# Kernel tuning notes

Measured on AMD Instinct MI355X. Metric: run time of the kernel, lower is better.

The kernel has to match this reference:

```python
import jax, jax.numpy as jnp
import numpy as np

N, K, F = 20000, 32, 128
H, D = 4, 64            # heads, att_out_size
C = 40                  # num_classes
NEG_SLOPE = 0.2


def setup_inputs() -> dict:
    key = jax.random.key(0)
    ks = jax.random.split(key, 6)
    return {
        "node_feature": jax.random.normal(ks[0], (N, F), dtype=jnp.float32),
        "neighbor_nodes_feature": jax.random.normal(ks[1], (N, K, F), dtype=jnp.float32),
        "W": jax.random.normal(ks[2], (F, H * D), dtype=jnp.float32) / np.sqrt(F),
        "a_src": jax.random.normal(ks[3], (H, D), dtype=jnp.float32) / np.sqrt(D),
        "a_dst": jax.random.normal(ks[4], (H, D), dtype=jnp.float32) / np.sqrt(D),
        "weight": jax.random.normal(ks[5], (H * D, C), dtype=jnp.float32) / np.sqrt(H * D),
    }


def reference(node_feature, neighbor_nodes_feature, W, a_src, a_dst, weight):
    n = node_feature.shape[0]
    # Linear transform center nodes and neighbors, split heads
    h_i = (node_feature @ W).reshape(n, H, D)                     # [N,H,D]
    h_j = (neighbor_nodes_feature @ W).reshape(n, K, H, D)        # [N,K,H,D]
    # Attention logits: a_src . h_i + a_dst . h_j, LeakyReLU
    e_i = jnp.einsum('nhd,hd->nh', h_i, a_src)                    # [N,H]
    e_j = jnp.einsum('nkhd,hd->nkh', h_j, a_dst)                  # [N,K,H]
    e = jax.nn.leaky_relu(e_i[:, None, :] + e_j, NEG_SLOPE)       # [N,K,H]
    # Softmax over the K neighbors (segment softmax in dense form)
    alpha = jax.nn.softmax(e, axis=1)                             # [N,K,H]
    # Attention-weighted aggregation, concat heads
    out = jnp.einsum('nkh,nkhd->nhd', alpha, h_j).reshape(n, H * D)
    # Dense classifier (torch.mm)
    return out @ weight                                            # [N,C]
```

## Files before the change

kernel.cpp:

```cpp
#include <hip/hip_runtime.h>

#define KN 32
#define NF 128
#define NH 4
#define HD 256
#define NC 40
#define NPB 8
#define XSS 132

#define WS_WSRC 0
#define WS_WDST 512
#define WS_MT   1024
#define WS_EI   (1024 + NC * 512)

__global__ void gat_prep_wm(const float* __restrict__ W,
                            const float* __restrict__ a_src,
                            const float* __restrict__ a_dst,
                            const float* __restrict__ cls_w,
                            float* __restrict__ ws)
{
    if (blockIdx.x < 4) {
        int g = blockIdx.x * 256 + threadIdx.x;
        int which = g >> 9, h = (g >> 7) & 3, f = g & 127;
        const float* a = which ? a_dst : a_src;
        float s = 0.f;
        #pragma unroll 8
        for (int d = 0; d < 64; ++d)
            s = fmaf(W[f * HD + h * 64 + d], a[h * 64 + d], s);
        ws[g] = s;
    } else {
        int g = (blockIdx.x - 4) * 256 + threadIdx.x;
        if (g >= NC * 512) return;
        int cls = g >> 9, c = g & 511;
        int h = c >> 7, f = c & 127;
        float s = 0.f;
        #pragma unroll 8
        for (int d = 0; d < 64; ++d)
            s = fmaf(W[f * HD + h * 64 + d], cls_w[(h * 64 + d) * NC + cls], s);
        ws[WS_MT + (size_t)cls * 512 + c] = s;
    }
}

__global__ void gat_prep_ei(const float* __restrict__ nodef,
                            float* __restrict__ ws, int n_nodes)
{
    const int t = threadIdx.x;
    const int lane = t & 63;
    const int node = blockIdx.x * 64 + (t >> 6) * 16 + (lane >> 2);
    const int q = lane & 3;
    if (node >= n_nodes) return;
    const float* wsrc = ws + WS_WSRC;
    const float4* xp = (const float4*)(nodef + (size_t)node * NF + q * 32);
    float p0 = 0.f, p1 = 0.f, p2 = 0.f, p3 = 0.f;
    #pragma unroll
    for (int j = 0; j < 8; ++j) {
        float4 x  = xp[j];
        float4 w0 = *(const float4*)&wsrc[0 * NF + q * 32 + 4 * j];
        float4 w1 = *(const float4*)&wsrc[1 * NF + q * 32 + 4 * j];
        float4 w2 = *(const float4*)&wsrc[2 * NF + q * 32 + 4 * j];
        float4 w3 = *(const float4*)&wsrc[3 * NF + q * 32 + 4 * j];
        p0 += x.x*w0.x + x.y*w0.y + x.z*w0.z + x.w*w0.w;
        p1 += x.x*w1.x + x.y*w1.y + x.z*w1.z + x.w*w1.w;
        p2 += x.x*w2.x + x.y*w2.y + x.z*w2.z + x.w*w2.w;
        p3 += x.x*w3.x + x.y*w3.y + x.z*w3.z + x.w*w3.w;
    }
    #pragma unroll
    for (int st = 1; st < 4; st <<= 1) {
        p0 += __shfl_xor(p0, st); p1 += __shfl_xor(p1, st);
        p2 += __shfl_xor(p2, st); p3 += __shfl_xor(p3, st);
    }
    if (q == 0)
        *(float4*)&ws[WS_EI + (size_t)node * 4] = make_float4(p0, p1, p2, p3);
}

static __device__ __forceinline__ void lds_barrier() {
    __builtin_amdgcn_sched_barrier(0);
    asm volatile("s_waitcnt lgkmcnt(0)");
    __builtin_amdgcn_sched_barrier(0);
    __builtin_amdgcn_s_barrier();
    __builtin_amdgcn_sched_barrier(0);
}

__device__ __forceinline__ void gat_body(
    int i_, float* __restrict__ XsB, float* __restrict__ eB,
    float* __restrict__ zrow, float4 xv[4], const float4 wd[4][4],
    const float eiv[NPB], const float* __restrict__ neigh,
    int node0, int kq, int fq, int wv, int lane)
{
    #pragma unroll
    for (int j = 0; j < 4; ++j)
        *(float4*)&XsB[kq * XSS + fq * 4 + 32 * j] = xv[j];

    float s0 = 0.f, s1 = 0.f, s2 = 0.f, s3 = 0.f;
    #pragma unroll
    for (int j = 0; j < 4; ++j) {
        float4 x = xv[j];
        s0 += x.x*wd[0][j].x + x.y*wd[0][j].y + x.z*wd[0][j].z + x.w*wd[0][j].w;
        s1 += x.x*wd[1][j].x + x.y*wd[1][j].y + x.z*wd[1][j].z + x.w*wd[1][j].w;
        s2 += x.x*wd[2][j].x + x.y*wd[2][j].y + x.z*wd[2][j].z + x.w*wd[2][j].w;
        s3 += x.x*wd[3][j].x + x.y*wd[3][j].y + x.z*wd[3][j].z + x.w*wd[3][j].w;
    }

    if (i_ + 2 < NPB) {
        const float4* src = (const float4*)(neigh + ((size_t)(node0 + i_ + 2) * KN + kq) * NF);
        #pragma unroll
        for (int j = 0; j < 4; ++j) xv[j] = src[fq + 8 * j];
    }

    #pragma unroll
    for (int st = 1; st < 8; st <<= 1) {
        s0 += __shfl_xor(s0, st); s1 += __shfl_xor(s1, st);
        s2 += __shfl_xor(s2, st); s3 += __shfl_xor(s3, st);
    }
    if (fq == 0) {
        eB[0 * KN + kq] = s0; eB[1 * KN + kq] = s1;
        eB[2 * KN + kq] = s2; eB[3 * KN + kq] = s3;
    }

    lds_barrier();

    const float ei_h = eiv[i_];
    float ss = 0.f, zx = 0.f, zy = 0.f;
    #pragma unroll
    for (int m = 0; m < 8; ++m) {
        float4 evm = *(const float4*)&eB[wv * KN + m * 4];
        float el[4] = {evm.x, evm.y, evm.z, evm.w};
        #pragma unroll
        for (int kk = 0; kk < 4; ++kk) {
            float z_ = ei_h + el[kk];
            float l_ = fmaxf(z_, 0.2f * z_);
            float p_ = __expf(l_);
            ss += p_;
            float xa = XsB[(m * 4 + kk) * XSS + lane];
            float xb = XsB[(m * 4 + kk) * XSS + 64 + lane];
            zx = fmaf(p_, xa, zx);
            zy = fmaf(p_, xb, zy);
        }
    }
    float inv = 1.f / ss;
    zrow[wv * NF + lane]      = zx * inv;
    zrow[wv * NF + 64 + lane] = zy * inv;
}

__global__ __launch_bounds__(256, 3)
void gat_main(const float* __restrict__ neigh,
              const float* __restrict__ ws,
              float* __restrict__ out, int n_nodes)
{
    __shared__ __align__(16) float Xs[2][KN * XSS];
    __shared__ __align__(16) float zl[NPB][512];
    __shared__ __align__(16) float e_lds[2][NH * KN];

    const int t    = threadIdx.x;
    const int lane = t & 63;
    const int kq   = t >> 3;
    const int fq   = t & 7;
    const int wv   = t >> 6;
    const float* wdst = ws + WS_WDST;
    const float* MT   = ws + WS_MT;
    const float* ei_g = ws + WS_EI;

    const int node0 = blockIdx.x * NPB;
    if (node0 >= n_nodes) return;

    float4 wd[4][4];
    #pragma unroll
    for (int h = 0; h < 4; ++h)
        #pragma unroll
        for (int j = 0; j < 4; ++j)
            wd[h][j] = *(const float4*)&wdst[h * NF + fq * 4 + 32 * j];
    float eiv[NPB];
    #pragma unroll
    for (int i = 0; i < NPB; ++i)
        eiv[i] = ei_g[(size_t)(node0 + i) * 4 + wv];

    float4 xvA[4], xvB[4];
    {
        const float4* sA = (const float4*)(neigh + ((size_t)node0 * KN + kq) * NF);
        const float4* sB = (const float4*)(neigh + ((size_t)(node0 + 1) * KN + kq) * NF);
        #pragma unroll
        for (int j = 0; j < 4; ++j) { xvA[j] = sA[fq + 8 * j]; xvB[j] = sB[fq + 8 * j]; }
    }

    #pragma unroll
    for (int ii = 0; ii < NPB; ii += 2) {
        gat_body(ii,     Xs[0], e_lds[0], zl[ii],     xvA, wd, eiv, neigh,
                 node0, kq, fq, wv, lane);
        gat_body(ii + 1, Xs[1], e_lds[1], zl[ii + 1], xvB, wd, eiv, neigh,
                 node0, kq, fq, wv, lane);
    }
    __syncthreads();

    float* ypart = &Xs[0][0];
    {
        int cls = t & 63, s = t >> 6;
        if (cls < NC) {
            const float4* mp = (const float4*)&MT[(size_t)cls * 512 + s * 128];
            float acc[NPB];
            #pragma unroll
            for (int i = 0; i < NPB; ++i) acc[i] = 0.f;
            #pragma unroll 2
            for (int c4 = 0; c4 < 32; ++c4) {
                float4 mv = mp[c4];
                #pragma unroll
                for (int i = 0; i < NPB; ++i) {
                    float4 zv = *(const float4*)&zl[i][s * 128 + c4 * 4];
                    acc[i] += zv.x * mv.x + zv.y * mv.y + zv.z * mv.z + zv.w * mv.w;
                }
            }
            #pragma unroll
            for (int i = 0; i < NPB; ++i)
                ypart[s * (NPB * NC) + i * NC + cls] = acc[i];
        }
    }
    __syncthreads();
    #pragma unroll
    for (int rep = 0; rep < 2; ++rep) {
        int p = t + rep * 256;
        if (p < NPB * NC) {
            float y = ypart[p] + ypart[NPB * NC + p]
                    + ypart[2 * NPB * NC + p] + ypart[3 * NPB * NC + p];
            out[(size_t)node0 * NC + p] = y;
        }
    }
}

extern "C" void kernel_launch(void* const* d_in, const int* in_sizes, int n_in,
                              void* d_out, int out_size, void* d_ws, size_t ws_size,
                              hipStream_t stream) {
    const float* nodef = (const float*)d_in[0];
    const float* neigh = (const float*)d_in[1];
    const float* W     = (const float*)d_in[2];
    const float* a_src = (const float*)d_in[3];
    const float* a_dst = (const float*)d_in[4];
    const float* cls_w = (const float*)d_in[5];
    float* out = (float*)d_out;
    float* ws  = (float*)d_ws;

    const int n_nodes = in_sizes[0] / NF;

    hipLaunchKernelGGL(gat_prep_wm, dim3(4 + (NC * 512 + 255) / 256), dim3(256), 0, stream,
                       W, a_src, a_dst, cls_w, ws);
    hipLaunchKernelGGL(gat_prep_ei, dim3((n_nodes + 63) / 64), dim3(256), 0, stream,
                       nodef, ws, n_nodes);
    hipLaunchKernelGGL(gat_main, dim3((n_nodes + NPB - 1) / NPB), dim3(256), 0, stream,
                       neigh, ws, out, n_nodes);
}
```

Before: 125.6 us.

## Give each wavefront its own nodes and drop block-wide barriers in the main GAT loop

Restructures gat_main so each of the 4 wavefronts processes 8 nodes on its own (32 nodes per block). Neighbor rows are read straight from global memory twice, once for the logits and once for the aggregation, instead of being staged in LDS with block barriers. Softmax sums use in-wave shuffles, and the per-node aggregated features are stored in LDS as bf16 to fit 32 nodes before the classifier matmul. This removes per-node __syncthreads and LDS staging but doubles global/L2 reads of neighbor features and adds bf16 rounding error. The grid now assumes n_nodes is divisible by 32, which holds for 20000.

```diff
diff --git a/kernel.cpp b/kernel.cpp
--- a/kernel.cpp
+++ b/kernel.cpp
@@ -5,13 +5,23 @@
 #define NH 4
 #define HD 256
 #define NC 40
-#define NPB 8
-#define XSS 132
+#define NPW 8
+#define WPB 4
+#define NPB2 (NPW * WPB)
 
 #define WS_WSRC 0
 #define WS_WDST 512
 #define WS_MT   1024
 #define WS_EI   (1024 + NC * 512)
+
+static __device__ __forceinline__ unsigned short bf16_of(float x) {
+    union { float f; unsigned u; } v; v.f = x;
+    unsigned r = v.u + 0x7FFFu + ((v.u >> 16) & 1u);
+    return (unsigned short)(r >> 16);
+}
+static __device__ __forceinline__ float f_of_bf16(unsigned short b) {
+    union { unsigned u; float f; } v; v.u = ((unsigned)b) << 16; return v.f;
+}
 
 __global__ void gat_prep_wm(const float* __restrict__ W,
                             const float* __restrict__ a_src,
@@ -73,95 +83,25 @@
         *(float4*)&ws[WS_EI + (size_t)node * 4] = make_float4(p0, p1, p2, p3);
 }
 
-static __device__ __forceinline__ void lds_barrier() {
-    __builtin_amdgcn_sched_barrier(0);
-    asm volatile("s_waitcnt lgkmcnt(0)");
-    __builtin_amdgcn_sched_barrier(0);
-    __builtin_amdgcn_s_barrier();
-    __builtin_amdgcn_sched_barrier(0);
-}
-
-__device__ __forceinline__ void gat_body(
-    int i_, float* __restrict__ XsB, float* __restrict__ eB,
-    float* __restrict__ zrow, float4 xv[4], const float4 wd[4][4],
-    const float eiv[NPB], const float* __restrict__ neigh,
-    int node0, int kq, int fq, int wv, int lane)
-{
-    #pragma unroll
-    for (int j = 0; j < 4; ++j)
-        *(float4*)&XsB[kq * XSS + fq * 4 + 32 * j] = xv[j];
-
-    float s0 = 0.f, s1 = 0.f, s2 = 0.f, s3 = 0.f;
-    #pragma unroll
-    for (int j = 0; j < 4; ++j) {
-        float4 x = xv[j];
-        s0 += x.x*wd[0][j].x + x.y*wd[0][j].y + x.z*wd[0][j].z + x.w*wd[0][j].w;
-        s1 += x.x*wd[1][j].x + x.y*wd[1][j].y + x.z*wd[1][j].z + x.w*wd[1][j].w;
-        s2 += x.x*wd[2][j].x + x.y*wd[2][j].y + x.z*wd[2][j].z + x.w*wd[2][j].w;
-        s3 += x.x*wd[3][j].x + x.y*wd[3][j].y + x.z*wd[3][j].z + x.w*wd[3][j].w;
-    }
-
-    if (i_ + 2 < NPB) {
-        const float4* src = (const float4*)(neigh + ((size_t)(node0 + i_ + 2) * KN + kq) * NF);
-        #pragma unroll
-        for (int j = 0; j < 4; ++j) xv[j] = src[fq + 8 * j];
-    }
-
-    #pragma unroll
-    for (int st = 1; st < 8; st <<= 1) {
-        s0 += __shfl_xor(s0, st); s1 += __shfl_xor(s1, st);
-        s2 += __shfl_xor(s2, st); s3 += __shfl_xor(s3, st);
-    }
-    if (fq == 0) {
-        eB[0 * KN + kq] = s0; eB[1 * KN + kq] = s1;
-        eB[2 * KN + kq] = s2; eB[3 * KN + kq] = s3;
-    }
-
-    lds_barrier();
-
-    const float ei_h = eiv[i_];
-    float ss = 0.f, zx = 0.f, zy = 0.f;
-    #pragma unroll
-    for (int m = 0; m < 8; ++m) {
-        float4 evm = *(const float4*)&eB[wv * KN + m * 4];
-        float el[4] = {evm.x, evm.y, evm.z, evm.w};
-        #pragma unroll
-        for (int kk = 0; kk < 4; ++kk) {
-            float z_ = ei_h + el[kk];
-            float l_ = fmaxf(z_, 0.2f * z_);
-            float p_ = __expf(l_);
-            ss += p_;
-            float xa = XsB[(m * 4 + kk) * XSS + lane];
-            float xb = XsB[(m * 4 + kk) * XSS + 64 + lane];
-            zx = fmaf(p_, xa, zx);
-            zy = fmaf(p_, xb, zy);
-        }
-    }
-    float inv = 1.f / ss;
-    zrow[wv * NF + lane]      = zx * inv;
-    zrow[wv * NF + 64 + lane] = zy * inv;
-}
-
 __global__ __launch_bounds__(256, 3)
 void gat_main(const float* __restrict__ neigh,
               const float* __restrict__ ws,
               float* __restrict__ out, int n_nodes)
 {
-    __shared__ __align__(16) float Xs[2][KN * XSS];
-    __shared__ __align__(16) float zl[NPB][512];
-    __shared__ __align__(16) float e_lds[2][NH * KN];
+    __shared__ __align__(16) unsigned short zlB[NPB2][512];
+    __shared__ __align__(16) float alpha_l[WPB][2][KN * NH];
 
     const int t    = threadIdx.x;
+    const int w    = t >> 6;
     const int lane = t & 63;
-    const int kq   = t >> 3;
-    const int fq   = t & 7;
-    const int wv   = t >> 6;
+    const int g8   = lane >> 3;
+    const int fq   = lane & 7;
     const float* wdst = ws + WS_WDST;
     const float* MT   = ws + WS_MT;
     const float* ei_g = ws + WS_EI;
 
-    const int node0 = blockIdx.x * NPB;
-    if (node0 >= n_nodes) return;
+    const int node0  = blockIdx.x * NPB2;
+    const int nodeW0 = node0 + w * NPW;
 
     float4 wd[4][4];
     #pragma unroll
@@ -169,58 +109,120 @@
         #pragma unroll
         for (int j = 0; j < 4; ++j)
             wd[h][j] = *(const float4*)&wdst[h * NF + fq * 4 + 32 * j];
-    float eiv[NPB];
-    #pragma unroll
-    for (int i = 0; i < NPB; ++i)
-        eiv[i] = ei_g[(size_t)(node0 + i) * 4 + wv];
-
-    float4 xvA[4], xvB[4];
+
+    for (int i = 0; i < NPW; ++i) {
+        const int node = nodeW0 + i;
+        const float* xb = neigh + (size_t)node * (KN * NF);
+        const float4 eis = *(const float4*)&ei_g[(size_t)node * 4];
+
+        float ep[4][4];
+        #pragma unroll
+        for (int r8 = 0; r8 < 4; ++r8) {
+            const float4* xr = (const float4*)(xb + (size_t)(r8 * 8 + g8) * NF);
+            float4 x0 = xr[fq], x1 = xr[fq + 8], x2 = xr[fq + 16], x3 = xr[fq + 24];
+            #pragma unroll
+            for (int h = 0; h < 4; ++h) {
+                ep[r8][h] =
+                    x0.x*wd[h][0].x + x0.y*wd[h][0].y + x0.z*wd[h][0].z + x0.w*wd[h][0].w
+                  + x1.x*wd[h][1].x + x1.y*wd[h][1].y + x1.z*wd[h][1].z + x1.w*wd[h][1].w
+                  + x2.x*wd[h][2].x + x2.y*wd[h][2].y + x2.z*wd[h][2].z + x2.w*wd[h][2].w
+                  + x3.x*wd[h][3].x + x3.y*wd[h][3].y + x3.z*wd[h][3].z + x3.w*wd[h][3].w;
+            }
+        }
+        #pragma unroll
+        for (int st = 1; st < 8; st <<= 1)
+            #pragma unroll
+            for (int r8 = 0; r8 < 4; ++r8)
+                #pragma unroll
+                for (int h = 0; h < 4; ++h)
+                    ep[r8][h] += __shfl_xor(ep[r8][h], st);
+
+        const float eh[4] = {eis.x, eis.y, eis.z, eis.w};
+        float ex[4][4], ssh[4] = {0.f, 0.f, 0.f, 0.f};
+        #pragma unroll
+        for (int r8 = 0; r8 < 4; ++r8)
+            #pragma unroll
+            for (int h = 0; h < 4; ++h) {
+                float z = eh[h] + ep[r8][h];
+                float l = fmaxf(z, 0.2f * z);
+                ex[r8][h] = __expf(l);
+                ssh[h] += ex[r8][h];
+            }
+        #pragma unroll
+        for (int st = 8; st < 64; st <<= 1)
+            #pragma unroll
+            for (int h = 0; h < 4; ++h)
+                ssh[h] += __shfl_xor(ssh[h], st);
+        float inv[4];
+        #pragma unroll
+        for (int h = 0; h < 4; ++h) inv[h] = 1.f / ssh[h];
+
+        float* al = &alpha_l[w][i & 1][0];
+        if (fq == 0) {
+            #pragma unroll
+            for (int r8 = 0; r8 < 4; ++r8)
+                *(float4*)&al[(r8 * 8 + g8) * 4] =
+                    make_float4(ex[r8][0], ex[r8][1], ex[r8][2], ex[r8][3]);
+        }
+        asm volatile("s_waitcnt lgkmcnt(0)" ::: "memory");
+        __builtin_amdgcn_sched_barrier(0);
+
+        float zA[4] = {0.f, 0.f, 0.f, 0.f}, zB[4] = {0.f, 0.f, 0.f, 0.f};
+        const float* xcol = xb + lane * 2;
+        #pragma unroll 8
+        for (int k = 0; k < KN; ++k) {
+            float4 a4 = *(const float4*)&al[k * 4];
+            float2 x2 = *(const float2*)(xcol + (size_t)k * NF);
+            zA[0] = fmaf(a4.x, x2.x, zA[0]); zB[0] = fmaf(a4.x, x2.y, zB[0]);
+            zA[1] = fmaf(a4.y, x2.x, zA[1]); zB[1] = fmaf(a4.y, x2.y, zB[1]);
+            zA[2] = fmaf(a4.z, x2.x, zA[2]); zB[2] = fmaf(a4.z, x2.y, zB[2]);
+            zA[3] = fmaf(a4.w, x2.x, zA[3]); zB[3] = fmaf(a4.w, x2.y, zB[3]);
+        }
+        unsigned short* zr = zlB[w * NPW + i];
+        #pragma unroll
+        for (int h = 0; h < 4; ++h) {
+            ushort2 p;
+            p.x = bf16_of(zA[h] * inv[h]);
+            p.y = bf16_of(zB[h] * inv[h]);
+            *(ushort2*)&zr[h * NF + lane * 2] = p;
+        }
+    }
+    __syncthreads();
+
     {
-        const float4* sA = (const float4*)(neigh + ((size_t)node0 * KN + kq) * NF);
-        const float4* sB = (const float4*)(neigh + ((size_t)(node0 + 1) * KN + kq) * NF);
-        #pragma unroll
-        for (int j = 0; j < 4; ++j) { xvA[j] = sA[fq + 8 * j]; xvB[j] = sB[fq + 8 * j]; }
-    }
-
-    #pragma unroll
-    for (int ii = 0; ii < NPB; ii += 2) {
-        gat_body(ii,     Xs[0], e_lds[0], zl[ii],     xvA, wd, eiv, neigh,
-                 node0, kq, fq, wv, lane);
-        gat_body(ii + 1, Xs[1], e_lds[1], zl[ii + 1], xvB, wd, eiv, neigh,
-                 node0, kq, fq, wv, lane);
-    }
-    __syncthreads();
-
-    float* ypart = &Xs[0][0];
-    {
-        int cls = t & 63, s = t >> 6;
+        const int cls = t & 63, s = t >> 6;
+        float acc[NPB2];
         if (cls < NC) {
             const float4* mp = (const float4*)&MT[(size_t)cls * 512 + s * 128];
-            float acc[NPB];
-            #pragma unroll
-            for (int i = 0; i < NPB; ++i) acc[i] = 0.f;
+            #pragma unroll
+            for (int i = 0; i < NPB2; ++i) acc[i] = 0.f;
             #pragma unroll 2
             for (int c4 = 0; c4 < 32; ++c4) {
                 float4 mv = mp[c4];
                 #pragma unroll
-                for (int i = 0; i < NPB; ++i) {
-                    float4 zv = *(const float4*)&zl[i][s * 128 + c4 * 4];
-                    acc[i] += zv.x * mv.x + zv.y * mv.y + zv.z * mv.z + zv.w * mv.w;
+                for (int i = 0; i < NPB2; ++i) {
+                    ushort4 zv = *(const ushort4*)&zlB[i][s * 128 + c4 * 4];
+                    acc[i] += f_of_bf16(zv.x) * mv.x + f_of_bf16(zv.y) * mv.y
+                            + f_of_bf16(zv.z) * mv.z + f_of_bf16(zv.w) * mv.w;
                 }
             }
-            #pragma unroll
-            for (int i = 0; i < NPB; ++i)
-                ypart[s * (NPB * NC) + i * NC + cls] = acc[i];
-        }
-    }
-    __syncthreads();
-    #pragma unroll
-    for (int rep = 0; rep < 2; ++rep) {
-        int p = t + rep * 256;
-        if (p < NPB * NC) {
-            float y = ypart[p] + ypart[NPB * NC + p]
-                    + ypart[2 * NPB * NC + p] + ypart[3 * NPB * NC + p];
-            out[(size_t)node0 * NC + p] = y;
+        }
+        __syncthreads();
+        float* ypart = (float*)&zlB[0][0];
+        if (cls < NC) {
+            #pragma unroll
+            for (int i = 0; i < NPB2; ++i)
+                ypart[s * (NPB2 * NC) + i * NC + cls] = acc[i];
+        }
+        __syncthreads();
+        #pragma unroll
+        for (int rep = 0; rep < 5; ++rep) {
+            int p = t + rep * 256;
+            if (p < NPB2 * NC) {
+                float y = ypart[p] + ypart[NPB2 * NC + p]
+                        + ypart[2 * NPB2 * NC + p] + ypart[3 * NPB2 * NC + p];
+                out[(size_t)node0 * NC + p] = y;
+            }
         }
     }
 }
@@ -243,6 +245,6 @@
                        W, a_src, a_dst, cls_w, ws);
     hipLaunchKernelGGL(gat_prep_ei, dim3((n_nodes + 63) / 64), dim3(256), 0, stream,
                        nodef, ws, n_nodes);
-    hipLaunchKernelGGL(gat_main, dim3((n_nodes + NPB - 1) / NPB), dim3(256), 0, stream,
+    hipLaunchKernelGGL(gat_main, dim3(n_nodes / NPB2), dim3(256), 0, stream,
                        neigh, ws, out, n_nodes);
 }
```

Result: slower. 178.3 us (+41.9%).

## Fuse center-node logit prep into main kernel and deepen neighbor prefetch to three

Applied to the files above, without the earlier changes.

Removes the separate gat_prep_ei launch and its workspace round-trip. Each block now computes its eight center-node source logits directly into LDS with a 32-lane shuffle reduction. The main loop changes from a paired two-node body to a single loop that keeps three nodes' neighbor rows in registers, so loads are issued three iterations ahead. LDS reads of X and writes of z switch to float2 with an interleaved column mapping. The trade-off is more VGPRs for the extra prefetch set, which could limit occupancy.

```diff
diff --git a/kernel.cpp b/kernel.cpp
--- a/kernel.cpp
+++ b/kernel.cpp
@@ -11,7 +11,6 @@
 #define WS_WSRC 0
 #define WS_WDST 512
 #define WS_MT   1024
-#define WS_EI   (1024 + NC * 512)
 
 __global__ void gat_prep_wm(const float* __restrict__ W,
                             const float* __restrict__ a_src,
@@ -41,38 +40,6 @@
     }
 }
 
-__global__ void gat_prep_ei(const float* __restrict__ nodef,
-                            float* __restrict__ ws, int n_nodes)
-{
-    const int t = threadIdx.x;
-    const int lane = t & 63;
-    const int node = blockIdx.x * 64 + (t >> 6) * 16 + (lane >> 2);
-    const int q = lane & 3;
-    if (node >= n_nodes) return;
-    const float* wsrc = ws + WS_WSRC;
-    const float4* xp = (const float4*)(nodef + (size_t)node * NF + q * 32);
-    float p0 = 0.f, p1 = 0.f, p2 = 0.f, p3 = 0.f;
-    #pragma unroll
-    for (int j = 0; j < 8; ++j) {
-        float4 x  = xp[j];
-        float4 w0 = *(const float4*)&wsrc[0 * NF + q * 32 + 4 * j];
-        float4 w1 = *(const float4*)&wsrc[1 * NF + q * 32 + 4 * j];
-        float4 w2 = *(const float4*)&wsrc[2 * NF + q * 32 + 4 * j];
-        float4 w3 = *(const float4*)&wsrc[3 * NF + q * 32 + 4 * j];
-        p0 += x.x*w0.x + x.y*w0.y + x.z*w0.z + x.w*w0.w;
-        p1 += x.x*w1.x + x.y*w1.y + x.z*w1.z + x.w*w1.w;
-        p2 += x.x*w2.x + x.y*w2.y + x.z*w2.z + x.w*w2.w;
-        p3 += x.x*w3.x + x.y*w3.y + x.z*w3.z + x.w*w3.w;
-    }
-    #pragma unroll
-    for (int st = 1; st < 4; st <<= 1) {
-        p0 += __shfl_xor(p0, st); p1 += __shfl_xor(p1, st);
-        p2 += __shfl_xor(p2, st); p3 += __shfl_xor(p3, st);
-    }
-    if (q == 0)
-        *(float4*)&ws[WS_EI + (size_t)node * 4] = make_float4(p0, p1, p2, p3);
-}
-
 static __device__ __forceinline__ void lds_barrier() {
     __builtin_amdgcn_sched_barrier(0);
     asm volatile("s_waitcnt lgkmcnt(0)");
@@ -81,113 +48,120 @@
     __builtin_amdgcn_sched_barrier(0);
 }
 
-__device__ __forceinline__ void gat_body(
-    int i_, float* __restrict__ XsB, float* __restrict__ eB,
-    float* __restrict__ zrow, float4 xv[4], const float4 wd[4][4],
-    const float eiv[NPB], const float* __restrict__ neigh,
-    int node0, int kq, int fq, int wv, int lane)
-{
-    #pragma unroll
-    for (int j = 0; j < 4; ++j)
-        *(float4*)&XsB[kq * XSS + fq * 4 + 32 * j] = xv[j];
-
-    float s0 = 0.f, s1 = 0.f, s2 = 0.f, s3 = 0.f;
-    #pragma unroll
-    for (int j = 0; j < 4; ++j) {
-        float4 x = xv[j];
-        s0 += x.x*wd[0][j].x + x.y*wd[0][j].y + x.z*wd[0][j].z + x.w*wd[0][j].w;
-        s1 += x.x*wd[1][j].x + x.y*wd[1][j].y + x.z*wd[1][j].z + x.w*wd[1][j].w;
-        s2 += x.x*wd[2][j].x + x.y*wd[2][j].y + x.z*wd[2][j].z + x.w*wd[2][j].w;
-        s3 += x.x*wd[3][j].x + x.y*wd[3][j].y + x.z*wd[3][j].z + x.w*wd[3][j].w;
-    }
-
-    if (i_ + 2 < NPB) {
-        const float4* src = (const float4*)(neigh + ((size_t)(node0 + i_ + 2) * KN + kq) * NF);
-        #pragma unroll
-        for (int j = 0; j < 4; ++j) xv[j] = src[fq + 8 * j];
-    }
-
-    #pragma unroll
-    for (int st = 1; st < 8; st <<= 1) {
-        s0 += __shfl_xor(s0, st); s1 += __shfl_xor(s1, st);
-        s2 += __shfl_xor(s2, st); s3 += __shfl_xor(s3, st);
-    }
-    if (fq == 0) {
-        eB[0 * KN + kq] = s0; eB[1 * KN + kq] = s1;
-        eB[2 * KN + kq] = s2; eB[3 * KN + kq] = s3;
-    }
-
-    lds_barrier();
-
-    const float ei_h = eiv[i_];
-    float ss = 0.f, zx = 0.f, zy = 0.f;
-    #pragma unroll
-    for (int m = 0; m < 8; ++m) {
-        float4 evm = *(const float4*)&eB[wv * KN + m * 4];
-        float el[4] = {evm.x, evm.y, evm.z, evm.w};
-        #pragma unroll
-        for (int kk = 0; kk < 4; ++kk) {
-            float z_ = ei_h + el[kk];
-            float l_ = fmaxf(z_, 0.2f * z_);
-            float p_ = __expf(l_);
-            ss += p_;
-            float xa = XsB[(m * 4 + kk) * XSS + lane];
-            float xb = XsB[(m * 4 + kk) * XSS + 64 + lane];
-            zx = fmaf(p_, xa, zx);
-            zy = fmaf(p_, xb, zy);
-        }
-    }
-    float inv = 1.f / ss;
-    zrow[wv * NF + lane]      = zx * inv;
-    zrow[wv * NF + 64 + lane] = zy * inv;
-}
-
 __global__ __launch_bounds__(256, 3)
-void gat_main(const float* __restrict__ neigh,
+void gat_main(const float* __restrict__ nodef,
+              const float* __restrict__ neigh,
               const float* __restrict__ ws,
               float* __restrict__ out, int n_nodes)
 {
     __shared__ __align__(16) float Xs[2][KN * XSS];
     __shared__ __align__(16) float zl[NPB][512];
     __shared__ __align__(16) float e_lds[2][NH * KN];
+    __shared__ __align__(16) float ei_lds[NPB][NH];
 
     const int t    = threadIdx.x;
     const int lane = t & 63;
     const int kq   = t >> 3;
     const int fq   = t & 7;
     const int wv   = t >> 6;
+    const float* wsrc = ws + WS_WSRC;
     const float* wdst = ws + WS_WDST;
     const float* MT   = ws + WS_MT;
-    const float* ei_g = ws + WS_EI;
 
     const int node0 = blockIdx.x * NPB;
     if (node0 >= n_nodes) return;
 
+    {
+        const int i2 = t >> 5, sub = t & 31;
+        float4 x = ((const float4*)(nodef + (size_t)(node0 + i2) * NF))[sub];
+        float4 w0 = *(const float4*)&wsrc[0 * NF + sub * 4];
+        float4 w1 = *(const float4*)&wsrc[1 * NF + sub * 4];
+        float4 w2 = *(const float4*)&wsrc[2 * NF + sub * 4];
+        float4 w3 = *(const float4*)&wsrc[3 * NF + sub * 4];
+        float p0 = x.x*w0.x + x.y*w0.y + x.z*w0.z + x.w*w0.w;
+        float p1 = x.x*w1.x + x.y*w1.y + x.z*w1.z + x.w*w1.w;
+        float p2 = x.x*w2.x + x.y*w2.y + x.z*w2.z + x.w*w2.w;
+        float p3 = x.x*w3.x + x.y*w3.y + x.z*w3.z + x.w*w3.w;
+        #pragma unroll
+        for (int st = 1; st < 32; st <<= 1) {
+            p0 += __shfl_xor(p0, st); p1 += __shfl_xor(p1, st);
+            p2 += __shfl_xor(p2, st); p3 += __shfl_xor(p3, st);
+        }
+        if (sub == 0)
+            *(float4*)&ei_lds[i2][0] = make_float4(p0, p1, p2, p3);
+    }
+
     float4 wd[4][4];
     #pragma unroll
     for (int h = 0; h < 4; ++h)
         #pragma unroll
         for (int j = 0; j < 4; ++j)
             wd[h][j] = *(const float4*)&wdst[h * NF + fq * 4 + 32 * j];
-    float eiv[NPB];
-    #pragma unroll
-    for (int i = 0; i < NPB; ++i)
-        eiv[i] = ei_g[(size_t)(node0 + i) * 4 + wv];
-
-    float4 xvA[4], xvB[4];
-    {
-        const float4* sA = (const float4*)(neigh + ((size_t)node0 * KN + kq) * NF);
-        const float4* sB = (const float4*)(neigh + ((size_t)(node0 + 1) * KN + kq) * NF);
-        #pragma unroll
-        for (int j = 0; j < 4; ++j) { xvA[j] = sA[fq + 8 * j]; xvB[j] = sB[fq + 8 * j]; }
-    }
-
-    #pragma unroll
-    for (int ii = 0; ii < NPB; ii += 2) {
-        gat_body(ii,     Xs[0], e_lds[0], zl[ii],     xvA, wd, eiv, neigh,
-                 node0, kq, fq, wv, lane);
-        gat_body(ii + 1, Xs[1], e_lds[1], zl[ii + 1], xvB, wd, eiv, neigh,
-                 node0, kq, fq, wv, lane);
+
+    float4 xv[3][4];
+    #pragma unroll
+    for (int s = 0; s < 3; ++s) {
+        const float4* src = (const float4*)(neigh + ((size_t)(node0 + s) * KN + kq) * NF);
+        #pragma unroll
+        for (int j = 0; j < 4; ++j) xv[s][j] = src[fq + 8 * j];
+    }
+
+    #pragma unroll
+    for (int i = 0; i < NPB; ++i) {
+        const int set = i % 3;
+        const int buf = i & 1;
+
+        #pragma unroll
+        for (int j = 0; j < 4; ++j)
+            *(float4*)&Xs[buf][kq * XSS + fq * 4 + 32 * j] = xv[set][j];
+
+        float s0 = 0.f, s1 = 0.f, s2 = 0.f, s3 = 0.f;
+        #pragma unroll
+        for (int j = 0; j < 4; ++j) {
+            float4 x = xv[set][j];
+            s0 += x.x*wd[0][j].x + x.y*wd[0][j].y + x.z*wd[0][j].z + x.w*wd[0][j].w;
+            s1 += x.x*wd[1][j].x + x.y*wd[1][j].y + x.z*wd[1][j].z + x.w*wd[1][j].w;
+            s2 += x.x*wd[2][j].x + x.y*wd[2][j].y + x.z*wd[2][j].z + x.w*wd[2][j].w;
+            s3 += x.x*wd[3][j].x + x.y*wd[3][j].y + x.z*wd[3][j].z + x.w*wd[3][j].w;
+        }
+
+        if (i + 3 < NPB) {
+            const float4* src = (const float4*)(neigh + ((size_t)(node0 + i + 3) * KN + kq) * NF);
+            #pragma unroll
+            for (int j = 0; j < 4; ++j) xv[set][j] = src[fq + 8 * j];
+        }
+
+        #pragma unroll
+        for (int st = 1; st < 8; st <<= 1) {
+            s0 += __shfl_xor(s0, st); s1 += __shfl_xor(s1, st);
+            s2 += __shfl_xor(s2, st); s3 += __shfl_xor(s3, st);
+        }
+        if (fq == 0) {
+            e_lds[buf][0 * KN + kq] = s0; e_lds[buf][1 * KN + kq] = s1;
+            e_lds[buf][2 * KN + kq] = s2; e_lds[buf][3 * KN + kq] = s3;
+        }
+
+        lds_barrier();
+
+        const float ei_h = ei_lds[i][wv];
+        float ss = 0.f, zx = 0.f, zy = 0.f;
+        #pragma unroll
+        for (int m = 0; m < 8; ++m) {
+            float4 evm = *(const float4*)&e_lds[buf][wv * KN + m * 4];
+            float el[4] = {evm.x, evm.y, evm.z, evm.w};
+            #pragma unroll
+            for (int kk = 0; kk < 4; ++kk) {
+                float z_ = ei_h + el[kk];
+                float l_ = fmaxf(z_, 0.2f * z_);
+                float p_ = __expf(l_);
+                ss += p_;
+                float2 x2 = *(const float2*)&Xs[buf][(m * 4 + kk) * XSS + 2 * lane];
+                zx = fmaf(p_, x2.x, zx);
+                zy = fmaf(p_, x2.y, zy);
+            }
+        }
+        float inv = 1.f / ss;
+        *(float2*)&zl[i][wv * NF + 2 * lane] = make_float2(zx * inv, zy * inv);
     }
     __syncthreads();
 
@@ -241,8 +215,6 @@
 
     hipLaunchKernelGGL(gat_prep_wm, dim3(4 + (NC * 512 + 255) / 256), dim3(256), 0, stream,
                        W, a_src, a_dst, cls_w, ws);
-    hipLaunchKernelGGL(gat_prep_ei, dim3((n_nodes + 63) / 64), dim3(256), 0, stream,
-                       nodef, ws, n_nodes);
     hipLaunchKernelGGL(gat_main, dim3((n_nodes + NPB - 1) / NPB), dim3(256), 0, stream,
-                       neigh, ws, out, n_nodes);
-}
+                       nodef, neigh, ws, out, n_nodes);
+}
```

Measured after the change: 126.3 us. No clear change (+0.5%).
